# Performance work log

Hardware: AMD Instinct MI355X
Metric: run time of the kernel (lower is better)

The kernel has to match this reference:

```python
import jax, jax.numpy as jnp
import numpy as np

B, OBS, ACT, NT, E = 4096, 512, 64, 10, 16
DREP, DH, DK = 1024, 1024, 512  # rep dim, expert hidden, key/value dim


def setup_inputs() -> dict:
    key = jax.random.key(0)
    ks = jax.random.split(key, 24)
    s = 0.02
    state_core = jax.random.normal(ks[0], (B, OBS), jnp.float32)
    task_ids = jax.random.randint(ks[1], (B,), 0, NT)
    onehot = jax.nn.one_hot(task_ids, NT, dtype=jnp.float32)
    state = jnp.concatenate([state_core, onehot], axis=-1)  # [B, OBS+NT]
    act = jax.random.normal(ks[2], (B, ACT), jnp.float32)
    return {
        "state": state,
        "act": act,
        "rep_W0": s * jax.random.normal(ks[3], (OBS + ACT, DREP), jnp.float32),
        "rep_b0": jnp.zeros((DREP,), jnp.float32),
        "rep_W1": s * jax.random.normal(ks[4], (DREP, DREP), jnp.float32),
        "rep_b1": jnp.zeros((DREP,), jnp.float32),
        "emb": 0.5 * jnp.ones((NT, DK), jnp.float32),
        "Wk0": s * jax.random.normal(ks[5], (E, DREP, DH), jnp.float32),
        "bk0": jnp.zeros((E, DH), jnp.float32),
        "Wk1": s * jax.random.normal(ks[6], (E, DH, DK), jnp.float32),
        "bk1": jnp.zeros((E, DK), jnp.float32),
        "Wv0": s * jax.random.normal(ks[7], (E, DREP, DH), jnp.float32),
        "bv0": jnp.zeros((E, DH), jnp.float32),
        "Wv1": s * jax.random.normal(ks[8], (E, DH, DK), jnp.float32),
        "bv1": jnp.zeros((E, DK), jnp.float32),
        "Wt0": s * jax.random.normal(ks[9], (DK, 512), jnp.float32),
        "bt0": jnp.zeros((512,), jnp.float32),
        "Wt1": s * jax.random.normal(ks[10], (512, 256), jnp.float32),
        "bt1": jnp.zeros((256,), jnp.float32),
        "Wt2": s * jax.random.normal(ks[11], (256, 1), jnp.float32),
        "bt2": jnp.zeros((1,), jnp.float32),
    }


def reference(state, act, rep_W0, rep_b0, rep_W1, rep_b1, emb,
              Wk0, bk0, Wk1, bk1, Wv0, bv0, Wv1, bv1,
              Wt0, bt0, Wt1, bt1, Wt2, bt2):
    num_tasks = emb.shape[0]
    task = jnp.argmax(state[:, -num_tasks:], axis=-1)  # one-hot -> index (== torch.nonzero)
    s = state[:, :-num_tasks]
    # representation: mlp([obs+act, 1024, 1024]) -> relu then identity
    x = jnp.concatenate([s, act], axis=-1)
    rep = jax.nn.relu(x @ rep_W0 + rep_b0) @ rep_W1 + rep_b1  # [B, DREP]
    query = jnp.tanh(emb[task])  # [B, DK]
    # all experts batched (original loops in Python over E tiny MLPs)
    hk = jax.nn.relu(jnp.einsum('bd,edh->ebh', rep, Wk0) + bk0[:, None, :])
    keys = jnp.einsum('ebh,ehk->ebk', hk, Wk1) + bk1[:, None, :]   # [E,B,DK]
    hv = jax.nn.relu(jnp.einsum('bd,edh->ebh', rep, Wv0) + bv0[:, None, :])
    vals = jnp.einsum('ebh,ehk->ebk', hv, Wv1) + bv1[:, None, :]   # [E,B,DK]
    logits = jnp.einsum('bk,ebk->be', query, keys)                 # [B,E]
    attn = jax.nn.softmax(logits, axis=1)
    tower_in = jnp.einsum('be,ebk->bk', attn, vals)                # [B,DK]
    h = jax.nn.relu(tower_in @ Wt0 + bt0)
    h = jax.nn.relu(h @ Wt1 + bt1)
    q = jnp.squeeze(h @ Wt2 + bt2, -1)                             # [B]
    expert_loss = -jnp.mean(
        jnp.sum(jnp.clip(jnp.log(attn + 1e-10), -6.0, 0.0), axis=-1) * 0.3)
    return q, expert_loss
```

## Files before the change

kernel.cpp:

```cpp
#include <hip/hip_runtime.h>
#include <cstdint>
#include <cstddef>

#define NB   4096
#define OBS  512
#define NACT 64
#define NT   10
#define NE   16
#define DREP 1024
#define DH   1024
#define DK   512
#define SLD  (OBS + NT)
#define XK   (OBS + NACT)

typedef short s8v __attribute__((ext_vector_type(8)));
typedef float f4v __attribute__((ext_vector_type(4)));

__device__ __forceinline__ unsigned short f2bf(float f) {
  union { float f; unsigned int u; } v; v.f = f;
  unsigned int u = v.u;
  unsigned int r = (u + 0x7FFFu + ((u >> 16) & 1u)) >> 16;
  return (unsigned short)r;
}
__device__ __forceinline__ float bf2f(unsigned short h) {
  union { unsigned int u; float f; } v; v.u = ((unsigned int)h) << 16;
  return v.f;
}

__device__ __forceinline__ void gload_lds16(const unsigned short* gp, const unsigned short* lp) {
  __builtin_amdgcn_global_load_lds(
      (const __attribute__((address_space(1))) void*)(uintptr_t)gp,
      (__attribute__((address_space(3))) void*)(unsigned int)(uintptr_t)lp,
      16, 0, 0);
}

template <int BM, int BN, int MODE, int RELU, int LDA, int LDB, int KK>
__global__ void __launch_bounds__(256)
gemm_k(const unsigned short* __restrict__ A,
       const unsigned short* __restrict__ Bt,
       const float* __restrict__ bias,
       unsigned short* __restrict__ outB, int ldo,
       const float* __restrict__ qk1, const int* __restrict__ task,
       float* __restrict__ logits, int eBase,
       const float* __restrict__ attn, float* __restrict__ cio)
{
  constexpr int FM = BM / 32;
  constexpr int FN = BN / 32;
  constexpr int CA = BM / 64;
  constexpr int CB = BN / 64;
  constexpr int NTILES = KK / 32;
  static_assert(NTILES >= 3, "pipeline depth");
  constexpr int LPS = CA + CB;
  static_assert(LPS < 16, "vmcnt immediate fits in low bits");
  constexpr int WAIT_STAGE = 0xF70 | LPS;
  constexpr int WAIT_ALL   = 0xF70;

  __shared__ __align__(16) unsigned short As[3][BM * 32];
  __shared__ __align__(16) unsigned short Bs[3][BN * 32];

  const int tid  = threadIdx.x;
  const int wave = tid >> 6;
  const int lane = tid & 63;
  const int wm = wave >> 1, wn = wave & 1;

  const int rowBase = blockIdx.x * BM;
  const int colBase = blockIdx.y * BN;

  if (MODE == 3 || MODE == 4) {
    A   += (size_t)blockIdx.z * KK;
    Bt  += (size_t)blockIdx.z * KK;
    cio += (size_t)blockIdx.z * NB * DK;
  }

  f4v acc[FM][FN];
#pragma unroll
  for (int m = 0; m < FM; ++m)
#pragma unroll
    for (int n = 0; n < FN; ++n) acc[m][n] = f4v{0.f, 0.f, 0.f, 0.f};

  const int sRow = lane >> 2;
  const int sSw  = ((lane & 3) ^ ((sRow >> 1) & 3)) * 8;

  const unsigned short* ag[CA];
  const unsigned short* bg[CB];
#pragma unroll
  for (int j = 0; j < CA; ++j)
    ag[j] = A + (size_t)(rowBase + (wave * CA + j) * 16 + sRow) * LDA + sSw;
#pragma unroll
  for (int j = 0; j < CB; ++j)
    bg[j] = Bt + (size_t)(colBase + (wave * CB + j) * 16 + sRow) * LDB + sSw;

  const int fr   = lane & 15;
  const int koSw = ((lane >> 4) ^ ((fr >> 1) & 3)) * 8;
  const int aOff = (wm * (BM / 2) + fr) * 32 + koSw;
  const int bOff = (wn * (BN / 2) + fr) * 32 + koSw;

  auto stage = [&](int buf) {
#pragma unroll
    for (int j = 0; j < CA; ++j) { gload_lds16(ag[j], &As[buf][(wave * CA + j) * 512]); ag[j] += 32; }
#pragma unroll
    for (int j = 0; j < CB; ++j) { gload_lds16(bg[j], &Bs[buf][(wave * CB + j) * 512]); bg[j] += 32; }
  };

  auto compute = [&](int buf) {
    s8v av[FM], bv[FN];
#pragma unroll
    for (int m = 0; m < FM; ++m)
      av[m] = *reinterpret_cast<const s8v*>(&As[buf][aOff + m * 512]);
#pragma unroll
    for (int n = 0; n < FN; ++n)
      bv[n] = *reinterpret_cast<const s8v*>(&Bs[buf][bOff + n * 512]);
#pragma unroll
    for (int m = 0; m < FM; ++m)
#pragma unroll
      for (int n = 0; n < FN; ++n)
        acc[m][n] = __builtin_amdgcn_mfma_f32_16x16x32_bf16(av[m], bv[n], acc[m][n], 0, 0, 0);
  };

  stage(0);
  stage(1);

  for (int t = 0; t < NTILES; t += 3) {
    if (t + 1 < NTILES) __builtin_amdgcn_s_waitcnt(WAIT_STAGE);
    else                __builtin_amdgcn_s_waitcnt(WAIT_ALL);
    __builtin_amdgcn_s_barrier();
    if (t + 2 < NTILES) stage(2);
    compute(0);
    if (t + 1 < NTILES) {
      if (t + 2 < NTILES) __builtin_amdgcn_s_waitcnt(WAIT_STAGE);
      else                __builtin_amdgcn_s_waitcnt(WAIT_ALL);
      __builtin_amdgcn_s_barrier();
      if (t + 3 < NTILES) stage(0);
      compute(1);
    }
    if (t + 2 < NTILES) {
      if (t + 3 < NTILES) __builtin_amdgcn_s_waitcnt(WAIT_STAGE);
      else                __builtin_amdgcn_s_waitcnt(WAIT_ALL);
      __builtin_amdgcn_s_barrier();
      if (t + 4 < NTILES) stage(1);
      compute(2);
    }
  }

  const int cr = (lane >> 4) * 4;
  const int cc = lane & 15;

  int gcn[FN];
  float bcol[FN];
#pragma unroll
  for (int n = 0; n < FN; ++n) {
    gcn[n] = colBase + wn * (BN / 2) + n * 16 + cc;
    bcol[n] = (MODE >= 3) ? 0.f : bias[gcn[n]];
  }

  if (MODE == 0) {
#pragma unroll
    for (int m = 0; m < FM; ++m)
#pragma unroll
      for (int r = 0; r < 4; ++r) {
        int gr = rowBase + wm * (BM / 2) + m * 16 + cr + r;
#pragma unroll
        for (int n = 0; n < FN; ++n) {
          float v = acc[m][n][r] + bcol[n];
          if (RELU) v = fmaxf(v, 0.f);
          outB[(size_t)gr * ldo + gcn[n]] = f2bf(v);
        }
      }
  }

  if (MODE == 3 || MODE == 4) {
#pragma unroll
    for (int m = 0; m < FM; ++m)
#pragma unroll
      for (int r = 0; r < 4; ++r) {
        int gr = rowBase + wm * (BM / 2) + m * 16 + cr + r;
#pragma unroll
        for (int n = 0; n < FN; ++n) {
          float v = acc[m][n][r];
          if (MODE == 4) v += cio[(size_t)gr * DK + gcn[n]];
          cio[(size_t)gr * DK + gcn[n]] = v;
        }
      }
  }
}

template <int MODE, int LDA, int LDB, int KK>
__global__ void __launch_bounds__(512)
gemm256_k(const unsigned short* __restrict__ A,
          const unsigned short* __restrict__ Bt,
          const float* __restrict__ bias,
          unsigned short* __restrict__ outB, int ldo,
          const float* __restrict__ qk1, const int* __restrict__ task,
          float* __restrict__ logits, int eBase,
          const float* __restrict__ attn)
{
  constexpr int NTK = KK / 64;
  static_assert(NTK >= 4 && (NTK & 1) == 0, "pipeline depth");

  __shared__ __align__(16) unsigned short As[2][16384];
  __shared__ __align__(16) unsigned short Bs[2][16384];

  const int tid  = threadIdx.x;
  const int wave = tid >> 6;
  const int lane = tid & 63;
  const int l3 = lane >> 3, l7 = lane & 7, l4 = lane >> 4;

  const int gx = gridDim.x, gy = gridDim.y;
  int flat = blockIdx.x + gx * (blockIdx.y + gy * blockIdx.z);
  const int nwg = gx * gy * gridDim.z;
  flat = (flat & 7) * (nwg >> 3) + (flat >> 3);
  const int bx = flat % gx; flat /= gx;
  const int by = flat % gy;
  const int bz = flat / gy;

  const int rowBase = bx * 256;
  const int colBase = by * 256;

  int eg = 0;
  if (MODE == 1) {
    eg = bz;
    Bt   += (size_t)eg * ((size_t)DREP * DH);
    bias += eg * DH;
    qk1  += (size_t)eg * (NT * DH);
  }
  if (MODE == 2) {
    eg = eBase + bz;
    Bt   += (size_t)eg * ((size_t)DREP * DH);
    bias += eg * DH;
    outB += (size_t)bz * DH;
  }

  f4v acc[2][2][2][4];
#pragma unroll
  for (int i0 = 0; i0 < 2; ++i0)
#pragma unroll
    for (int i1 = 0; i1 < 2; ++i1)
#pragma unroll
      for (int i2 = 0; i2 < 2; ++i2)
#pragma unroll
        for (int i3 = 0; i3 < 4; ++i3)
          acc[i0][i1][i2][i3] = f4v{0.f, 0.f, 0.f, 0.f};

  const unsigned short* pA[2][2];
  const unsigned short* pB[2][2];
#pragma unroll
  for (int h = 0; h < 2; ++h)
#pragma unroll
    for (int j = 0; j < 2; ++j) {
      const int r  = h * 128 + j * 64 + wave * 8 + l3;
      const int ks = (l7 ^ l3) * 8;
      pA[h][j] = A  + (size_t)(rowBase + r) * LDA + ks;
      pB[h][j] = Bt + (size_t)(colBase + r) * LDB + ks;
    }

  auto stageA = [&](int buf, int h) {
#pragma unroll
    for (int j = 0; j < 2; ++j) {
      gload_lds16(pA[h][j], &As[buf][h * 8192 + j * 4096 + wave * 512]);
      pA[h][j] += 64;
    }
  };
  auto stageB = [&](int buf, int h) {
#pragma unroll
    for (int j = 0; j < 2; ++j) {
      gload_lds16(pB[h][j], &Bs[buf][h * 8192 + j * 4096 + wave * 512]);
      pB[h][j] += 64;
    }
  };

  const int cOff0 = (l4 ^ l7) * 8;
  const int cOff1 = ((4 + l4) ^ l7) * 8;
  const int aRowOff = ((wave & 3) * 32 + (lane & 15)) * 64;
  const int bColOff = ((wave >> 2) * 64 + (lane & 15)) * 64;

  s8v avA[2][2], avB[2][2], bv[4][2];
  auto readAh = [&](int buf, int h, s8v (&av)[2][2]) {
#pragma unroll
    for (int f = 0; f < 2; ++f) {
      const unsigned short* p = &As[buf][h * 8192 + aRowOff + f * 1024];
      av[f][0] = *reinterpret_cast<const s8v*>(p + cOff0);
      av[f][1] = *reinterpret_cast<const s8v*>(p + cOff1);
    }
  };
  auto readB = [&](int buf, int qn) {
#pragma unroll
    for (int fc = 0; fc < 4; ++fc) {
      const unsigned short* p = &Bs[buf][qn * 8192 + bColOff + fc * 1024];
      bv[fc][0] = *reinterpret_cast<const s8v*>(p + cOff0);
      bv[fc][1] = *reinterpret_cast<const s8v*>(p + cOff1);
    }
  };

#define MFMA_BLK(QM, QN, AV)                                                  \
  do {                                                                        \
    __builtin_amdgcn_s_setprio(1);                                            \
    _Pragma("unroll") for (int ks_ = 0; ks_ < 2; ++ks_)                       \
      _Pragma("unroll") for (int f_ = 0; f_ < 2; ++f_)                        \
        _Pragma("unroll") for (int fc_ = 0; fc_ < 4; ++fc_)                   \
          acc[QM][QN][f_][fc_] = __builtin_amdgcn_mfma_f32_16x16x32_bf16(     \
              AV[f_][ks_], bv[fc_][ks_], acc[QM][QN][f_][fc_], 0, 0, 0);      \
    __builtin_amdgcn_s_setprio(0);                                            \
  } while (0)

  auto tile_body = [&](int t, int buf) __attribute__((always_inline)) {
    readAh(buf, 1, avB);
    if (t + 1 < NTK) {
      stageA(buf ^ 1, 0); stageB(buf ^ 1, 0);
      stageA(buf ^ 1, 1); stageB(buf ^ 1, 1);
    }
    MFMA_BLK(0, 0, avA);
    MFMA_BLK(1, 0, avB);
    readB(buf, 1);
    MFMA_BLK(1, 1, avB);
    MFMA_BLK(0, 1, avA);
    if (t + 1 < NTK) {
      __builtin_amdgcn_s_waitcnt(0xF70);
      __builtin_amdgcn_s_barrier();
      readAh(buf ^ 1, 0, avA);
      readB(buf ^ 1, 0);
    }
  };

  stageA(0, 0); stageB(0, 0); stageA(0, 1); stageB(0, 1);
  __builtin_amdgcn_s_waitcnt(0xF70);
  __builtin_amdgcn_s_barrier();
  readAh(0, 0, avA);
  readB(0, 0);

  for (int t = 0; t < NTK; t += 2) {
    tile_body(t, 0);
    tile_body(t + 1, 1);
  }
#undef MFMA_BLK

  const int cr = l4 * 4;
  const int cc = lane & 15;

  int gcn[2][4];
  float bcol[2][4];
#pragma unroll
  for (int qn = 0; qn < 2; ++qn)
#pragma unroll
    for (int fc = 0; fc < 4; ++fc) {
      gcn[qn][fc]  = colBase + qn * 128 + (wave >> 2) * 64 + fc * 16 + cc;
      bcol[qn][fc] = bias[gcn[qn][fc]];
    }

  if (MODE == 1) {
#pragma unroll
    for (int qm = 0; qm < 2; ++qm)
#pragma unroll
      for (int f = 0; f < 2; ++f)
#pragma unroll
        for (int r = 0; r < 4; ++r) {
          const int gr = rowBase + qm * 128 + (wave & 3) * 32 + f * 16 + cr + r;
          const float* qrow = qk1 + (size_t)task[gr] * DH;
          float s = 0.f;
#pragma unroll
          for (int qn = 0; qn < 2; ++qn)
#pragma unroll
            for (int fc = 0; fc < 4; ++fc) {
              float v = fmaxf(acc[qm][qn][f][fc][r] + bcol[qn][fc], 0.f);
              s += v * qrow[gcn[qn][fc]];
            }
#pragma unroll
          for (int off = 1; off < 16; off <<= 1) s += __shfl_xor(s, off, 64);
          if (cc == 0) atomicAdd(&logits[gr * NE + eg], s);
        }
  }

  if (MODE == 2) {
#pragma unroll
    for (int qm = 0; qm < 2; ++qm)
#pragma unroll
      for (int f = 0; f < 2; ++f)
#pragma unroll
        for (int r = 0; r < 4; ++r) {
          const int gr = rowBase + qm * 128 + (wave & 3) * 32 + f * 16 + cr + r;
          const float aw = attn[gr * NE + eg];
#pragma unroll
          for (int qn = 0; qn < 2; ++qn)
#pragma unroll
            for (int fc = 0; fc < 4; ++fc) {
              float v = fmaxf(acc[qm][qn][f][fc][r] + bcol[qn][fc], 0.f) * aw;
              outB[(size_t)gr * ldo + gcn[qn][fc]] = f2bf(v);
            }
        }
  }
}

__global__ void __launch_bounds__(256)
front_k(const float* __restrict__ state, const float* __restrict__ act,
        const float* __restrict__ emb, const float* __restrict__ bk1,
        unsigned short* __restrict__ x, int* __restrict__ task,
        float* __restrict__ Qt, float* __restrict__ qb)
{
  const int blk = blockIdx.x, tid = threadIdx.x;
  if (blk < 16) {
    int b = blk * 256 + tid;
    const float* p = state + (size_t)b * SLD + OBS;
    float best = p[0]; int bi = 0;
    for (int j = 1; j < NT; ++j) { float v = p[j]; if (v > best) { best = v; bi = j; } }
    task[b] = bi;
  } else if (blk < 16 + 1152) {
    int idx8 = (blk - 16) * 256 + tid;
    int b = idx8 / 72, c8 = idx8 - b * 72, j = c8 * 8;
    float v[8];
    if (j < OBS) {
      const float* s = state + (size_t)b * SLD + j;
#pragma unroll
      for (int q = 0; q < 8; ++q) v[q] = s[q];
    } else {
      const float* a = act + (size_t)b * NACT + (j - OBS);
#pragma unroll
      for (int q = 0; q < 8; ++q) v[q] = a[q];
    }
    unsigned short v8[8];
#pragma unroll
    for (int q = 0; q < 8; ++q) v8[q] = f2bf(v[q]);
    *reinterpret_cast<s8v*>(x + (size_t)b * XK + j) = *reinterpret_cast<const s8v*>(v8);
  } else if (blk < 16 + 1152 + 40) {
    int w = (blk - 1168) * 4 + (tid >> 6), lane = tid & 63;
    int e = w / NT, t = w - e * NT;
    const float* ep = emb + t * DK + lane * 8;
    const float* bp = bk1 + e * DK + lane * 8;
    float s = 0.f;
#pragma unroll
    for (int q = 0; q < 8; ++q) s += tanhf(ep[q]) * bp[q];
    for (int off = 1; off < 64; off <<= 1) s += __shfl_xor(s, off, 64);
    if (lane == 0) qb[e * NT + t] = s;
  } else {
    int idx = (blk - 1208) * 256 + tid;
    Qt[idx] = tanhf(emb[idx]);
  }
}

__global__ void qk1_k(const float* __restrict__ Wk1, const float* __restrict__ Qt,
                      float* __restrict__ qk1) {
  int w = (blockIdx.x * blockDim.x + threadIdx.x) >> 6;
  int lane = threadIdx.x & 63;
  if (w >= NE * DH) return;
  int e = w >> 10, h = w & (DH - 1);
  const float* wrow = Wk1 + ((size_t)e * DH + h) * DK + lane * 8;
  float wv[8];
#pragma unroll
  for (int j = 0; j < 8; ++j) wv[j] = wrow[j];
#pragma unroll
  for (int t = 0; t < NT; ++t) {
    const float* qrow = Qt + t * DK + lane * 8;
    float s = 0.f;
#pragma unroll
    for (int j = 0; j < 8; ++j) s += wv[j] * qrow[j];
#pragma unroll
    for (int off = 1; off < 64; off <<= 1) s += __shfl_xor(s, off, 64);
    if (lane == 0) qk1[((size_t)e * NT + t) * DH + h] = s;
  }
}

__global__ void __launch_bounds__(256)
convT_all_k(const float* __restrict__ W0,  unsigned short* __restrict__ dW0,
            const float* __restrict__ W1,  unsigned short* __restrict__ dW1,
            const float* __restrict__ Wk0, unsigned short* __restrict__ dWk0,
            const float* __restrict__ Wv0, unsigned short* __restrict__ dWv0,
            const float* __restrict__ Wv1, unsigned short* __restrict__ dWv1,
            const float* __restrict__ Wt0, unsigned short* __restrict__ dWt0,
            const float* __restrict__ Wt1, unsigned short* __restrict__ dWt1)
{
  int id = blockIdx.x;
  const float* src; unsigned short* dst;
  int N, dLd, nx, tpe; long sBS, dBS;
  if (id < 144)        {            src = W0;  dst = dW0;  N = 1024; sBS = 0; dBS = 0; dLd = 576;   nx = 16; tpe = 144; }
  else if (id < 400)   { id -= 144; src = W1;  dst = dW1;  N = 1024; sBS = 0; dBS = 0; dLd = 1024;  nx = 16; tpe = 256; }
  else if (id < 4496)  { id -= 400; src = Wk0; dst = dWk0; N = 1024; sBS = (long)DREP * DH; dBS = (long)DREP * DH; dLd = 1024; nx = 16; tpe = 256; }
  else if (id < 8592)  { id -= 4496; src = Wv0; dst = dWv0; N = 1024; sBS = (long)DREP * DH; dBS = (long)DREP * DH; dLd = 1024; nx = 16; tpe = 256; }
  else if (id < 10640) { id -= 8592; src = Wv1; dst = dWv1; N = 512;  sBS = (long)DH * DK; dBS = 1024; dLd = NE * DH; nx = 8; tpe = 128; }
  else if (id < 10704) { id -= 10640; src = Wt0; dst = dWt0; N = 512; sBS = 0; dBS = 0; dLd = 512; nx = 8; tpe = 64; }
  else                 { id -= 10704; src = Wt1; dst = dWt1; N = 256; sBS = 0; dBS = 0; dLd = 512; nx = 4; tpe = 32; }
  const int e  = id / tpe;
  const int r  = id - e * tpe;
  const int n0 = (r % nx) * 64, k0 = (r / nx) * 64;

  __shared__ float tile[64][65];
  src += (size_t)e * sBS + (size_t)k0 * N + n0;
  dst += (size_t)e * dBS + (size_t)n0 * dLd + k0;
  int t = threadIdx.x;
  int c4 = t & 15, kr = t >> 4;
#pragma unroll
  for (int i = 0; i < 4; ++i) {
    float4 v = *(const float4*)(src + (size_t)(kr + i * 16) * N + c4 * 4);
    tile[kr + i * 16][c4 * 4 + 0] = v.x;
    tile[kr + i * 16][c4 * 4 + 1] = v.y;
    tile[kr + i * 16][c4 * 4 + 2] = v.z;
    tile[kr + i * 16][c4 * 4 + 3] = v.w;
  }
  __syncthreads();
  int sub = t & 7, nl = t >> 3;
#pragma unroll
  for (int pass = 0; pass < 2; ++pass) {
    int n = nl + pass * 32;
    unsigned short v8[8];
#pragma unroll
    for (int j = 0; j < 8; ++j) v8[j] = f2bf(tile[sub * 8 + j][n]);
    *reinterpret_cast<s8v*>(dst + (size_t)n * dLd + sub * 8) =
        *reinterpret_cast<const s8v*>(v8);
  }
}

__global__ void __launch_bounds__(256)
attn_k(const float* __restrict__ logits, const float* __restrict__ qb,
       const int* __restrict__ task, const float* __restrict__ bv1,
       float* __restrict__ attn, float* __restrict__ twin,
       float* __restrict__ lossOut)
{
  __shared__ float aL[16][16];
  __shared__ float lred[4];
  const int tid = threadIdx.x;
  const int rr = tid >> 4, e = tid & 15;
  const int b = blockIdx.x * 16 + rr;
  const int t = task[b];
  float l = logits[b * NE + e] + qb[e * NT + t];
  float mx = l;
#pragma unroll
  for (int off = 1; off < 16; off <<= 1) mx = fmaxf(mx, __shfl_xor(mx, off, 64));
  float ex = expf(l - mx);
  float s = ex;
#pragma unroll
  for (int off = 1; off < 16; off <<= 1) s += __shfl_xor(s, off, 64);
  float a = ex / s;
  attn[b * NE + e] = a;
  aL[rr][e] = a;
  float loss = fminf(fmaxf(logf(a + 1e-10f), -6.f), 0.f);
#pragma unroll
  for (int off = 1; off < 64; off <<= 1) loss += __shfl_xor(loss, off, 64);
  if ((tid & 63) == 0) lred[tid >> 6] = loss;
  __syncthreads();
  if (tid == 0)
    atomicAdd(lossOut, (lred[0] + lred[1] + lred[2] + lred[3]) * (-0.3f / NB));
  float av[NE];
#pragma unroll
  for (int q = 0; q < NE; ++q) av[q] = aL[rr][q];
  float* tw = twin + (size_t)b * DK;
  for (int j = 0; j < 32; ++j) {
    int k = e + j * 16;
    float sv = 0.f;
#pragma unroll
    for (int q = 0; q < NE; ++q) sv += av[q] * bv1[q * DK + k];
    tw[k] = sv;
  }
}

__global__ void cvt_ti_k(const float* __restrict__ twin, const float* __restrict__ P,
                         unsigned short* __restrict__ ti) {
  int idx = (blockIdx.x * blockDim.x + threadIdx.x) * 8;
  if (idx >= NB * DK) return;
  float v[8];
#pragma unroll
  for (int j = 0; j < 8; ++j) v[j] = twin[idx + j];
#pragma unroll
  for (int c = 0; c < 4; ++c) {
    const float* p = P + (size_t)c * NB * DK + idx;
#pragma unroll
    for (int j = 0; j < 8; ++j) v[j] += p[j];
  }
  unsigned short v8[8];
#pragma unroll
  for (int j = 0; j < 8; ++j) v8[j] = f2bf(v[j]);
  *reinterpret_cast<s8v*>(ti + idx) = *reinterpret_cast<const s8v*>(v8);
}

__global__ void qfinal_k(const unsigned short* __restrict__ h2, const float* __restrict__ Wt2,
                         const float* __restrict__ bt2, float* __restrict__ out) {
  int w = (blockIdx.x * blockDim.x + threadIdx.x) >> 6;
  int lane = threadIdx.x & 63;
  if (w >= NB) return;
  float s = 0.f;
#pragma unroll
  for (int j = 0; j < 4; ++j) {
    int k = lane * 4 + j;
    s += bf2f(h2[(size_t)w * 256 + k]) * Wt2[k];
  }
  for (int off = 1; off < 64; off <<= 1) s += __shfl_xor(s, off, 64);
  if (lane == 0) out[w] = s + bt2[0];
}

extern "C" void kernel_launch(void* const* d_in, const int* in_sizes, int n_in,
                              void* d_out, int out_size, void* d_ws, size_t ws_size,
                              hipStream_t stream) {
  const float* state  = (const float*)d_in[0];
  const float* act    = (const float*)d_in[1];
  const float* rep_W0 = (const float*)d_in[2];
  const float* rep_b0 = (const float*)d_in[3];
  const float* rep_W1 = (const float*)d_in[4];
  const float* rep_b1 = (const float*)d_in[5];
  const float* emb    = (const float*)d_in[6];
  const float* Wk0    = (const float*)d_in[7];
  const float* bk0    = (const float*)d_in[8];
  const float* Wk1    = (const float*)d_in[9];
  const float* bk1    = (const float*)d_in[10];
  const float* Wv0    = (const float*)d_in[11];
  const float* bv0    = (const float*)d_in[12];
  const float* Wv1    = (const float*)d_in[13];
  const float* bv1    = (const float*)d_in[14];
  const float* Wt0    = (const float*)d_in[15];
  const float* bt0    = (const float*)d_in[16];
  const float* Wt1    = (const float*)d_in[17];
  const float* bt1    = (const float*)d_in[18];
  const float* Wt2    = (const float*)d_in[19];
  const float* bt2    = (const float*)d_in[20];
  float* out = (float*)d_out;

  char* wsb = (char*)d_ws;
  size_t off = 0;
  auto alloc = [&](size_t bytes) -> void* {
    void* p = wsb + off;
    off += (bytes + 255) & ~(size_t)255;
    return p;
  };
  unsigned short* Ap    = (unsigned short*)alloc((size_t)NB * 8192 * 2);
  unsigned short* Wk0t  = (unsigned short*)alloc((size_t)NE * DREP * DH * 2);
  unsigned short* Wv0t  = (unsigned short*)alloc((size_t)NE * DREP * DH * 2);
  unsigned short* Wv1t  = (unsigned short*)alloc((size_t)DK * (NE * DH) * 2);
  float*          P     = (float*)alloc((size_t)4 * NB * DK * 4);
  unsigned short* h0    = (unsigned short*)alloc((size_t)NB * DREP * 2);
  unsigned short* rep   = (unsigned short*)alloc((size_t)NB * DREP * 2);
  float*          twin  = (float*)alloc((size_t)NB * DK * 4);
  unsigned short* xbuf  = (unsigned short*)alloc((size_t)NB * XK * 2);
  unsigned short* ti    = (unsigned short*)alloc((size_t)NB * DK * 2);
  unsigned short* h1    = (unsigned short*)alloc((size_t)NB * 512 * 2);
  unsigned short* h2    = (unsigned short*)alloc((size_t)NB * 256 * 2);
  unsigned short* rW1t  = (unsigned short*)alloc((size_t)DREP * DREP * 2);
  unsigned short* rW0t  = (unsigned short*)alloc((size_t)DREP * XK * 2);
  float*          qk1   = (float*)alloc((size_t)NE * NT * DH * 4);
  unsigned short* Wt0t  = (unsigned short*)alloc((size_t)512 * 512 * 2);
  unsigned short* Wt1t  = (unsigned short*)alloc((size_t)256 * 512 * 2);
  float*          logits= (float*)alloc((size_t)NB * NE * 4);
  float*          attn  = (float*)alloc((size_t)NB * NE * 4);
  float*          Qt    = (float*)alloc((size_t)NT * DK * 4);
  int*            task  = (int*)alloc((size_t)NB * 4);
  float*          qb    = (float*)alloc((size_t)NE * NT * 4);

  hipMemsetAsync(logits, 0, (size_t)NB * NE * 4, stream);
  hipMemsetAsync(out + NB, 0, sizeof(float), stream);

  front_k<<<1228, 256, 0, stream>>>(state, act, emb, bk1, xbuf, task, Qt, qb);
  qk1_k<<<NE * DH / 4, 256, 0, stream>>>(Wk1, Qt, qk1);

  convT_all_k<<<10736, 256, 0, stream>>>(rep_W0, rW0t, rep_W1, rW1t,
                                         Wk0, Wk0t, Wv0, Wv0t, Wv1, Wv1t,
                                         Wt0, Wt0t, Wt1, Wt1t);

  gemm_k<128, 128, 0, 1, XK, XK, XK><<<dim3(NB / 128, DREP / 128, 1), 256, 0, stream>>>(
      xbuf, rW0t, rep_b0, h0, DREP, nullptr, nullptr, nullptr, 0, nullptr, nullptr);
  gemm_k<128, 128, 0, 0, DREP, DREP, DREP><<<dim3(NB / 128, DREP / 128, 1), 256, 0, stream>>>(
      h0, rW1t, rep_b1, rep, DREP, nullptr, nullptr, nullptr, 0, nullptr, nullptr);

  gemm256_k<1, DREP, DREP, DREP><<<dim3(NB / 256, DH / 256, NE), 512, 0, stream>>>(
      rep, Wk0t, bk0, nullptr, 0, qk1, task, logits, 0, nullptr);

  attn_k<<<NB / 16, 256, 0, stream>>>(logits, qb, task, bv1, attn, twin, out + NB);

  for (int g = 0; g < 2; ++g) {
    gemm256_k<2, DREP, DREP, DREP><<<dim3(NB / 256, DH / 256, 8), 512, 0, stream>>>(
        rep, Wv0t, bv0, Ap, 8192, nullptr, nullptr, nullptr, g * 8, attn);
    if (g == 0)
      gemm_k<128, 128, 3, 0, 8192, NE * DH, 2048><<<dim3(NB / 128, DK / 128, 4), 256, 0, stream>>>(
          Ap, Wv1t, nullptr, nullptr, 0, nullptr, nullptr, nullptr, 0, nullptr, P);
    else
      gemm_k<128, 128, 4, 0, 8192, NE * DH, 2048><<<dim3(NB / 128, DK / 128, 4), 256, 0, stream>>>(
          Ap, Wv1t + (size_t)8192, nullptr, nullptr, 0, nullptr, nullptr, nullptr, 0, nullptr, P);
  }
  cvt_ti_k<<<(NB * DK / 8 + 255) / 256, 256, 0, stream>>>(twin, P, ti);

  gemm_k<64, 64, 0, 1, DK, DK, DK><<<dim3(NB / 64, 512 / 64, 1), 256, 0, stream>>>(
      ti, Wt0t, bt0, h1, 512, nullptr, nullptr, nullptr, 0, nullptr, nullptr);
  gemm_k<64, 64, 0, 1, 512, 512, 512><<<dim3(NB / 64, 256 / 64, 1), 256, 0, stream>>>(
      h1, Wt1t, bt1, h2, 256, nullptr, nullptr, nullptr, 0, nullptr, nullptr);
  qfinal_k<<<NB / 4, 256, 0, stream>>>(h2, Wt2, bt2, out);
}
```

Before: 716.5 us.

## Switch 256x256 GEMM to 32x32x16 MFMA with per-wave 64x128 subtiles

Replaces the 16x16x32 bf16 MFMA tiling in the main expert GEMM kernel with 32x32x16 MFMAs. Each wave now owns a contiguous 64x128 output subtile instead of four scattered quadrants. The LDS read schedule is restructured: A fragments for all k-steps are loaded once, B is split into two halves, and the A and B global-to-LDS staging is interleaved between the MFMA groups. The intent is fewer LDS fragment reads per FLOP and higher MFMA throughput, at the cost of different register pressure and wider 32-lane reductions in the fused logits epilogue.

```diff
diff --git a/kernel.cpp b/kernel.cpp
--- a/kernel.cpp
+++ b/kernel.cpp
@@ -15,6 +15,7 @@
 
 typedef short s8v __attribute__((ext_vector_type(8)));
 typedef float f4v __attribute__((ext_vector_type(4)));
+typedef float f16vt __attribute__((ext_vector_type(16)));
 
 __device__ __forceinline__ unsigned short f2bf(float f) {
   union { float f; unsigned int u; } v; v.f = f;
@@ -203,7 +204,7 @@
   const int tid  = threadIdx.x;
   const int wave = tid >> 6;
   const int lane = tid & 63;
-  const int l3 = lane >> 3, l7 = lane & 7, l4 = lane >> 4;
+  const int l3 = lane >> 3, l7 = lane & 7, l5 = lane >> 5, l31 = lane & 31;
 
   const int gx = gridDim.x, gy = gridDim.y;
   int flat = blockIdx.x + gx * (blockIdx.y + gy * blockIdx.z);
@@ -230,16 +231,13 @@
     outB += (size_t)bz * DH;
   }
 
-  f4v acc[2][2][2][4];
+  f16vt acc[2][4];
 #pragma unroll
   for (int i0 = 0; i0 < 2; ++i0)
 #pragma unroll
-    for (int i1 = 0; i1 < 2; ++i1)
-#pragma unroll
-      for (int i2 = 0; i2 < 2; ++i2)
-#pragma unroll
-        for (int i3 = 0; i3 < 4; ++i3)
-          acc[i0][i1][i2][i3] = f4v{0.f, 0.f, 0.f, 0.f};
+    for (int i1 = 0; i1 < 4; ++i1)
+#pragma unroll
+      for (int i2 = 0; i2 < 16; ++i2) acc[i0][i1][i2] = 0.f;
 
   const unsigned short* pA[2][2];
   const unsigned short* pB[2][2];
@@ -268,124 +266,120 @@
     }
   };
 
-  const int cOff0 = (l4 ^ l7) * 8;
-  const int cOff1 = ((4 + l4) ^ l7) * 8;
-  const int aRowOff = ((wave & 3) * 32 + (lane & 15)) * 64;
-  const int bColOff = ((wave >> 2) * 64 + (lane & 15)) * 64;
-
-  s8v avA[2][2], avB[2][2], bv[4][2];
-  auto readAh = [&](int buf, int h, s8v (&av)[2][2]) {
-#pragma unroll
-    for (int f = 0; f < 2; ++f) {
-      const unsigned short* p = &As[buf][h * 8192 + aRowOff + f * 1024];
-      av[f][0] = *reinterpret_cast<const s8v*>(p + cOff0);
-      av[f][1] = *reinterpret_cast<const s8v*>(p + cOff1);
-    }
-  };
-  auto readB = [&](int buf, int qn) {
-#pragma unroll
-    for (int fc = 0; fc < 4; ++fc) {
-      const unsigned short* p = &Bs[buf][qn * 8192 + bColOff + fc * 1024];
-      bv[fc][0] = *reinterpret_cast<const s8v*>(p + cOff0);
-      bv[fc][1] = *reinterpret_cast<const s8v*>(p + cOff1);
-    }
-  };
-
-#define MFMA_BLK(QM, QN, AV)                                                  \
+  int cSw[4];
+#pragma unroll
+  for (int ks = 0; ks < 4; ++ks) cSw[ks] = ((ks * 2 + l5) ^ l7) * 8;
+  const int aBase = ((wave & 3) * 64 + l31) * 64;
+  const int bBase = ((wave >> 2) * 128 + l31) * 64;
+
+  s8v av[2][4];
+  s8v bK[4][2];
+  s8v bL[4][2];
+
+  auto readA_all = [&](int buf) {
+#pragma unroll
+    for (int mf = 0; mf < 2; ++mf)
+#pragma unroll
+      for (int ks = 0; ks < 4; ++ks)
+        av[mf][ks] = *reinterpret_cast<const s8v*>(&As[buf][aBase + mf * 2048 + cSw[ks]]);
+  };
+  auto readB01 = [&](int buf) {
+#pragma unroll
+    for (int nf = 0; nf < 4; ++nf)
+#pragma unroll
+      for (int ks = 0; ks < 2; ++ks)
+        bK[nf][ks] = *reinterpret_cast<const s8v*>(&Bs[buf][bBase + nf * 2048 + cSw[ks]]);
+  };
+  auto readB23 = [&](int buf) {
+#pragma unroll
+    for (int nf = 0; nf < 4; ++nf)
+#pragma unroll
+      for (int j = 0; j < 2; ++j)
+        bL[nf][j] = *reinterpret_cast<const s8v*>(&Bs[buf][bBase + nf * 2048 + cSw[2 + j]]);
+  };
+
+#define MFMA_KS(KS, BV, BI)                                                   \
   do {                                                                        \
-    __builtin_amdgcn_s_setprio(1);                                            \
-    _Pragma("unroll") for (int ks_ = 0; ks_ < 2; ++ks_)                       \
-      _Pragma("unroll") for (int f_ = 0; f_ < 2; ++f_)                        \
-        _Pragma("unroll") for (int fc_ = 0; fc_ < 4; ++fc_)                   \
-          acc[QM][QN][f_][fc_] = __builtin_amdgcn_mfma_f32_16x16x32_bf16(     \
-              AV[f_][ks_], bv[fc_][ks_], acc[QM][QN][f_][fc_], 0, 0, 0);      \
-    __builtin_amdgcn_s_setprio(0);                                            \
+    _Pragma("unroll") for (int mf_ = 0; mf_ < 2; ++mf_)                       \
+      _Pragma("unroll") for (int nf_ = 0; nf_ < 4; ++nf_)                     \
+        acc[mf_][nf_] = __builtin_amdgcn_mfma_f32_32x32x16_bf16(              \
+            av[mf_][KS], BV[nf_][BI], acc[mf_][nf_], 0, 0, 0);                \
   } while (0)
 
   auto tile_body = [&](int t, int buf) __attribute__((always_inline)) {
-    readAh(buf, 1, avB);
-    if (t + 1 < NTK) {
-      stageA(buf ^ 1, 0); stageB(buf ^ 1, 0);
-      stageA(buf ^ 1, 1); stageB(buf ^ 1, 1);
-    }
-    MFMA_BLK(0, 0, avA);
-    MFMA_BLK(1, 0, avB);
-    readB(buf, 1);
-    MFMA_BLK(1, 1, avB);
-    MFMA_BLK(0, 1, avA);
+    readB23(buf);
+    if (t + 1 < NTK) { stageA(buf ^ 1, 0); stageA(buf ^ 1, 1); }
+    __builtin_amdgcn_s_setprio(1);
+    MFMA_KS(0, bK, 0);
+    MFMA_KS(1, bK, 1);
+    __builtin_amdgcn_s_setprio(0);
+    if (t + 1 < NTK) { stageB(buf ^ 1, 0); stageB(buf ^ 1, 1); }
+    __builtin_amdgcn_s_setprio(1);
+    MFMA_KS(2, bL, 0);
+    MFMA_KS(3, bL, 1);
+    __builtin_amdgcn_s_setprio(0);
     if (t + 1 < NTK) {
       __builtin_amdgcn_s_waitcnt(0xF70);
       __builtin_amdgcn_s_barrier();
-      readAh(buf ^ 1, 0, avA);
-      readB(buf ^ 1, 0);
+      readB01(buf ^ 1);
+      readA_all(buf ^ 1);
     }
   };
 
   stageA(0, 0); stageB(0, 0); stageA(0, 1); stageB(0, 1);
   __builtin_amdgcn_s_waitcnt(0xF70);
   __builtin_amdgcn_s_barrier();
-  readAh(0, 0, avA);
-  readB(0, 0);
+  readB01(0);
+  readA_all(0);
 
   for (int t = 0; t < NTK; t += 2) {
     tile_body(t, 0);
     tile_body(t + 1, 1);
   }
-#undef MFMA_BLK
-
-  const int cr = l4 * 4;
-  const int cc = lane & 15;
-
-  int gcn[2][4];
-  float bcol[2][4];
-#pragma unroll
-  for (int qn = 0; qn < 2; ++qn)
-#pragma unroll
-    for (int fc = 0; fc < 4; ++fc) {
-      gcn[qn][fc]  = colBase + qn * 128 + (wave >> 2) * 64 + fc * 16 + cc;
-      bcol[qn][fc] = bias[gcn[qn][fc]];
-    }
+#undef MFMA_KS
+
+  int gcn[4];
+  float bcol[4];
+#pragma unroll
+  for (int nf = 0; nf < 4; ++nf) {
+    gcn[nf]  = colBase + (wave >> 2) * 128 + nf * 32 + l31;
+    bcol[nf] = bias[gcn[nf]];
+  }
 
   if (MODE == 1) {
 #pragma unroll
-    for (int qm = 0; qm < 2; ++qm)
-#pragma unroll
-      for (int f = 0; f < 2; ++f)
-#pragma unroll
-        for (int r = 0; r < 4; ++r) {
-          const int gr = rowBase + qm * 128 + (wave & 3) * 32 + f * 16 + cr + r;
-          const float* qrow = qk1 + (size_t)task[gr] * DH;
-          float s = 0.f;
-#pragma unroll
-          for (int qn = 0; qn < 2; ++qn)
-#pragma unroll
-            for (int fc = 0; fc < 4; ++fc) {
-              float v = fmaxf(acc[qm][qn][f][fc][r] + bcol[qn][fc], 0.f);
-              s += v * qrow[gcn[qn][fc]];
-            }
-#pragma unroll
-          for (int off = 1; off < 16; off <<= 1) s += __shfl_xor(s, off, 64);
-          if (cc == 0) atomicAdd(&logits[gr * NE + eg], s);
+    for (int mf = 0; mf < 2; ++mf)
+#pragma unroll
+      for (int r = 0; r < 16; ++r) {
+        const int gr = rowBase + (wave & 3) * 64 + mf * 32 +
+                       (r & 3) + 8 * (r >> 2) + 4 * l5;
+        const float* qrow = qk1 + (size_t)task[gr] * DH;
+        float s = 0.f;
+#pragma unroll
+        for (int nf = 0; nf < 4; ++nf) {
+          float v = fmaxf(acc[mf][nf][r] + bcol[nf], 0.f);
+          s += v * qrow[gcn[nf]];
         }
+#pragma unroll
+        for (int off = 1; off < 32; off <<= 1) s += __shfl_xor(s, off, 64);
+        if (l31 == 0) atomicAdd(&logits[gr * NE + eg], s);
+      }
   }
 
   if (MODE == 2) {
 #pragma unroll
-    for (int qm = 0; qm < 2; ++qm)
-#pragma unroll
-      for (int f = 0; f < 2; ++f)
-#pragma unroll
-        for (int r = 0; r < 4; ++r) {
-          const int gr = rowBase + qm * 128 + (wave & 3) * 32 + f * 16 + cr + r;
-          const float aw = attn[gr * NE + eg];
-#pragma unroll
-          for (int qn = 0; qn < 2; ++qn)
-#pragma unroll
-            for (int fc = 0; fc < 4; ++fc) {
-              float v = fmaxf(acc[qm][qn][f][fc][r] + bcol[qn][fc], 0.f) * aw;
-              outB[(size_t)gr * ldo + gcn[qn][fc]] = f2bf(v);
-            }
+    for (int mf = 0; mf < 2; ++mf)
+#pragma unroll
+      for (int r = 0; r < 16; ++r) {
+        const int gr = rowBase + (wave & 3) * 64 + mf * 32 +
+                       (r & 3) + 8 * (r >> 2) + 4 * l5;
+        const float aw = attn[gr * NE + eg];
+#pragma unroll
+        for (int nf = 0; nf < 4; ++nf) {
+          float v = fmaxf(acc[mf][nf][r] + bcol[nf], 0.f) * aw;
+          outB[(size_t)gr * ldo + gcn[nf]] = f2bf(v);
         }
+      }
   }
 }
 
```

Result: slower. 899.8 us (+25.6%).
